# Kernel optimization log

Hardware: AMD Instinct MI355X
Metric: run time of the kernel (lower is better)

Reference implementation:

```python
import jax, jax.numpy as jnp
import numpy as np

N, T, H, W, C = 4, 8, 64, 64, 512
WS = 8  # window size; H, W are exact multiples so pad/depad are identity


def setup_inputs() -> dict:
    key = jax.random.key(0)
    k1, k2, k3, k4 = jax.random.split(key, 4)
    x = jax.random.normal(k1, (N, T, H, W, C), dtype=jnp.float32)
    local_pos_embed = jax.random.normal(k2, (WS, WS, C), dtype=jnp.float32)
    W_in = jax.random.normal(k3, (3 * C, C), dtype=jnp.float32) * 0.02
    b_in = jnp.zeros((3 * C,), dtype=jnp.float32)
    W_out = jax.random.normal(k4, (C, C), dtype=jnp.float32) * 0.02
    b_out = jnp.zeros((C,), dtype=jnp.float32)
    return {"x": x, "local_pos_embed": local_pos_embed, "W_in": W_in,
            "b_in": b_in, "W_out": W_out, "b_out": b_out, "num_heads": 8}


def reference(x, local_pos_embed, W_in, b_in, W_out, b_out, num_heads):
    n, t, h, w, c = x.shape
    ws = local_pos_embed.shape[0]
    nh, nw = h // ws, w // ws
    head_dim = c // num_heads
    scale = 1.0 / jnp.sqrt(jnp.asarray(head_dim, dtype=x.dtype))

    # window partition: (N*T, H, W, C) -> (N*T*nh*nw, ws*ws, C)
    xw = x.reshape(n * t, nh, ws, nw, ws, c)
    xw = xw.transpose(0, 1, 3, 2, 4, 5).reshape(n * t * nh * nw, ws * ws, c)

    pos = local_pos_embed.reshape(ws * ws, c)  # flatten(0,1)
    qk_in = xw + pos[None, :, :]               # pos added to q,k only

    Wq, Wk, Wv = W_in[:c], W_in[c:2 * c], W_in[2 * c:]
    bq, bk, bv = b_in[:c], b_in[c:2 * c], b_in[2 * c:]

    B, S = qk_in.shape[0], qk_in.shape[1]
    q = (qk_in @ Wq.T + bq).reshape(B, S, num_heads, head_dim)
    k = (qk_in @ Wk.T + bk).reshape(B, S, num_heads, head_dim)
    v = (xw @ Wv.T + bv).reshape(B, S, num_heads, head_dim)

    scores = jnp.einsum('bqhd,bkhd->bhqk', q * scale, k)
    attn = jax.nn.softmax(scores, axis=-1)
    out = jnp.einsum('bhqk,bkhd->bqhd', attn, v).reshape(B, S, c)
    out = out @ W_out.T + b_out

    # reverse window partition
    out = out.reshape(n * t, nh, nw, ws, ws, c)
    out = out.transpose(0, 1, 3, 2, 4, 5).reshape(n, t, h, w, c)
    return out
```

## Files before the change

kernel.cpp:

```cpp
#include <hip/hip_runtime.h>

typedef _Float16 f16;
typedef unsigned int u32;
typedef f16 f16x8 __attribute__((ext_vector_type(8)));
typedef f16 f16x4 __attribute__((ext_vector_type(4)));
typedef float f32x4 __attribute__((ext_vector_type(4)));


__device__ __forceinline__ int src_row(int m) {
    int win = m >> 6, s = m & 63;
    return ((win >> 6) << 12) | (((win >> 3) & 7) << 9) | ((s >> 3) << 6) |
           ((win & 7) << 3) | (s & 7);
}

__device__ __forceinline__ void gload_lds16(const void* g, void* lds) {
    __builtin_amdgcn_global_load_lds(
        (const __attribute__((address_space(1))) u32*)g,
        (__attribute__((address_space(3))) u32*)lds, 16, 0, 0);
}

__device__ __forceinline__ f16* sp(char* S, int r, int c) {
    return (f16*)(S + r * 1024 + ((c * 2) ^ ((r & 7) << 4)));
}

__global__ __launch_bounds__(256) void prep_weights_k(
        const float* __restrict__ Wi, const float* __restrict__ Wo,
        f16* __restrict__ Wi_h, f16* __restrict__ Wo_h) {
    int i = blockIdx.x * 256 + threadIdx.x;
    const float4* src;
    f16* dst;
    int idx;
    if (i < 196608) { src = (const float4*)Wi; dst = Wi_h; idx = i; }
    else            { src = (const float4*)Wo; dst = Wo_h; idx = i - 196608; }
    float4 v = src[idx];
    f16x4 h = {(f16)v.x, (f16)v.y, (f16)v.z, (f16)v.w};
    *(f16x4*)(dst + (size_t)idx * 4) = h;
}

__global__ __launch_bounds__(256) void prep_bias_k(
        const float* __restrict__ pos, const float* __restrict__ Wi,
        const float* __restrict__ b_in, float* __restrict__ biasT) {
    int idx = blockIdx.x * 256 + threadIdx.x;
    int s = idx / 1536, o = idx % 1536;
    float acc = b_in[o];
    if (o < 1024) {
        const float4* p4 = (const float4*)(pos + (size_t)s * 512);
        const float4* w4 = (const float4*)(Wi + (size_t)o * 512);
        #pragma unroll 4
        for (int c = 0; c < 128; ++c) {
            float4 a = p4[c], b = w4[c];
            acc += a.x * b.x + a.y * b.y + a.z * b.z + a.w * b.w;
        }
    }
    biasT[idx] = acc;
}

__global__ __launch_bounds__(256) void prep_x_k(
        const float* __restrict__ x, f16* __restrict__ xh, int m0) {
    int i = blockIdx.x * 256 + threadIdx.x;
    int ml = i >> 6, c8 = (i & 63) * 8;
    int sr = src_row(m0 + ml);
    const float4* s4 = (const float4*)(x + (size_t)sr * 512 + c8);
    float4 a = s4[0], b = s4[1];
    f16x8 hv = {(f16)a.x, (f16)a.y, (f16)a.z, (f16)a.w,
                (f16)b.x, (f16)b.y, (f16)b.z, (f16)b.w};
    *(f16x8*)(xh + (size_t)ml * 512 + c8) = hv;
}

__global__ void __launch_bounds__(512, 2) qkv_gemm8_k(
        const f16* __restrict__ xh, const f16* __restrict__ Wh,
        const float* __restrict__ biasT, f16* __restrict__ qkv, int nblk) {
    extern __shared__ f16 lds[];
    int tid = threadIdx.x;
    int lane = tid & 63, wid = tid >> 6;
    int l15 = lane & 15, g = lane >> 4;
    int wm = wid >> 2, wn = wid & 3;
    int sid = (blockIdx.x & 7) * (nblk >> 3) + (blockIdx.x >> 3);
    int bm = sid / 6, bn = sid % 6;
    const f16* Ap = xh + (size_t)bm * 256 * 512;
    const f16* Bp = Wh + (size_t)bn * 256 * 512;

    int li0 = tid, li1 = tid + 512;
    int r0 = li0 >> 3, c0 = li0 & 7, r1 = li1 >> 3, c1 = li1 & 7;
    int off0 = r0 * 512 + ((c0 ^ (r0 & 7)) * 8);
    int off1 = r1 * 512 + ((c1 ^ (r1 & 7)) * 8);

    auto stage = [&](const f16* panel, int ldsbase, int tt, int h) {
        int tb = tt & 1;
        int dst = ldsbase + (tb * 2 + h) * 8192 + wid * 512;
        const f16* src = panel + h * 65536 + tt * 64;
        gload_lds16(src + off0, (void*)&lds[dst]);
        gload_lds16(src + off1, (void*)&lds[dst + 4096]);
    };

    f32x4 acc[8][4];
    f32x4 zero4 = {0.f, 0.f, 0.f, 0.f};
    #pragma unroll
    for (int a = 0; a < 8; ++a)
        #pragma unroll
        for (int b = 0; b < 4; ++b) acc[a][b] = zero4;
    f16x8 bf[4][2];

    stage(Ap, 0, 0, 0); stage(Ap, 0, 0, 1);
    stage(Bp, 32768, 0, 0); stage(Bp, 32768, 0, 1);
    stage(Ap, 0, 1, 0); stage(Ap, 0, 1, 1);
    stage(Bp, 32768, 1, 0); stage(Bp, 32768, 1, 1);
    asm volatile("s_waitcnt vmcnt(0)" ::: "memory");
    __builtin_amdgcn_s_barrier();

    #pragma unroll
    for (int tt = 0; tt < 8; ++tt) {
        int tb = tt & 1;
        const f16* Ab = &lds[(tb * 2 + wm) * 8192];
        const f16* Bb = &lds[32768 + (tb * 2 + (wn >> 1)) * 8192];
        #pragma unroll
        for (int q = 0; q < 4; ++q) {
            f16x8 af[2][2];
            #pragma unroll
            for (int ml = 0; ml < 2; ++ml) {
                int rr = (q * 2 + ml) * 16 + l15;
                #pragma unroll
                for (int ks = 0; ks < 2; ++ks)
                    af[ml][ks] = *(const f16x8*)&Ab[rr * 64 + (((ks * 4 + g) ^ (rr & 7)) * 8)];
            }
            if (q == 0) {
                #pragma unroll
                for (int nf = 0; nf < 4; ++nf) {
                    int rb = (wn & 1) * 64 + nf * 16 + l15;
                    #pragma unroll
                    for (int ks = 0; ks < 2; ++ks)
                        bf[nf][ks] = *(const f16x8*)&Bb[rb * 64 + (((ks * 4 + g) ^ (rb & 7)) * 8)];
                }
            }
            if (q <= 1) {
                if ((tt & 1) ? (tt + 1 < 8) : (tt >= 2)) stage(Ap, 0, tt + 1, q);
            } else {
                if (tt + 2 < 8) stage(Bp, 32768, tt + 2, q - 2);
            }
            __builtin_amdgcn_s_barrier();
            __builtin_amdgcn_s_setprio(1);
            #pragma unroll
            for (int ml = 0; ml < 2; ++ml)
                #pragma unroll
                for (int nf = 0; nf < 4; ++nf)
                    #pragma unroll
                    for (int ks = 0; ks < 2; ++ks)
                        acc[q * 2 + ml][nf] = __builtin_amdgcn_mfma_f32_16x16x32_f16(
                            af[ml][ks], bf[nf][ks], acc[q * 2 + ml][nf], 0, 0, 0);
            __builtin_amdgcn_s_setprio(0);
            if (q == 3) {
                if (tt < 6)       asm volatile("s_waitcnt vmcnt(4)" ::: "memory");
                else if (tt == 6) asm volatile("s_waitcnt vmcnt(0)" ::: "memory");
            }
            __builtin_amdgcn_s_barrier();
        }
    }

    int browg = bm * 256 + wm * 128, bcolg = bn * 256 + wn * 64;
    #pragma unroll
    for (int mf = 0; mf < 8; ++mf) {
        #pragma unroll
        for (int nf = 0; nf < 4; ++nf) {
            int col = bcolg + nf * 16 + l15;
            #pragma unroll
            for (int j = 0; j < 4; ++j) {
                int row = browg + mf * 16 + g * 4 + j;
                float v = acc[mf][nf][j] + biasT[(row & 63) * 1536 + col];
                qkv[(size_t)row * 1536 + col] = (f16)v;
            }
        }
    }
}

__global__ __launch_bounds__(512) void attn_k(
        const f16* __restrict__ qkv, f16* __restrict__ attn_h) {
    __shared__ __align__(16) char S[64 * 1024];
    int tid = threadIdx.x;
    int lane = tid & 63, h = tid >> 6;
    int l15 = lane & 15, g = lane >> 4;
    const f16* base = qkv + (size_t)blockIdx.x * 64 * 1536;
    int qc = h * 64, kc = 512 + h * 64, vc = 1024 + h * 64;

    f32x4 zero4 = {0.f, 0.f, 0.f, 0.f};
    f32x4 acc[4][4];
    #pragma unroll
    for (int a = 0; a < 4; ++a)
        #pragma unroll
        for (int b = 0; b < 4; ++b) acc[a][b] = zero4;

    {
        f16x8 qf[4][2], kf[4][2];
        #pragma unroll
        for (int mf = 0; mf < 4; ++mf)
            #pragma unroll
            for (int ks = 0; ks < 2; ++ks)
                qf[mf][ks] = *reinterpret_cast<const f16x8*>(base + (size_t)(mf * 16 + l15) * 1536 + qc + ks * 32 + g * 8);
        #pragma unroll
        for (int nf = 0; nf < 4; ++nf)
            #pragma unroll
            for (int ks = 0; ks < 2; ++ks)
                kf[nf][ks] = *reinterpret_cast<const f16x8*>(base + (size_t)(nf * 16 + l15) * 1536 + kc + ks * 32 + g * 8);
        #pragma unroll
        for (int ks = 0; ks < 2; ++ks)
            #pragma unroll
            for (int mf = 0; mf < 4; ++mf)
                #pragma unroll
                for (int nf = 0; nf < 4; ++nf)
                    acc[mf][nf] = __builtin_amdgcn_mfma_f32_16x16x32_f16(qf[mf][ks], kf[nf][ks], acc[mf][nf], 0, 0, 0);
    }

    f16x8 vf[4][2];
    #pragma unroll
    for (int nf = 0; nf < 4; ++nf)
        #pragma unroll
        for (int ks = 0; ks < 2; ++ks) {
            f16x8 v;
            #pragma unroll
            for (int j = 0; j < 8; ++j)
                v[j] = base[(size_t)(ks * 32 + g * 8 + j) * 1536 + vc + nf * 16 + l15];
            vf[nf][ks] = v;
        }

    char* Sh = S + h * 8192;
    #pragma unroll
    for (int mf = 0; mf < 4; ++mf) {
        #pragma unroll
        for (int j = 0; j < 4; ++j) {
            float mx = -1e30f;
            #pragma unroll
            for (int nf = 0; nf < 4; ++nf) mx = fmaxf(mx, acc[mf][nf][j]);
            #pragma unroll
            for (int off = 1; off < 16; off <<= 1) mx = fmaxf(mx, __shfl_xor(mx, off));
            float e[4], sum = 0.f;
            #pragma unroll
            for (int nf = 0; nf < 4; ++nf) {
                e[nf] = __expf((acc[mf][nf][j] - mx) * 0.125f);
                sum += e[nf];
            }
            #pragma unroll
            for (int off = 1; off < 16; off <<= 1) sum += __shfl_xor(sum, off);
            float rinv = __fdividef(1.0f, sum);
            int row = mf * 16 + g * 4 + j;
            #pragma unroll
            for (int nf = 0; nf < 4; ++nf)
                *(f16*)(Sh + row * 128 + (((nf * 16 + l15) * 2) ^ ((row & 7) << 4))) = (f16)(e[nf] * rinv);
        }
    }

    f32x4 acc2[4][4];
    #pragma unroll
    for (int a = 0; a < 4; ++a)
        #pragma unroll
        for (int b = 0; b < 4; ++b) acc2[a][b] = zero4;
    #pragma unroll
    for (int ks = 0; ks < 2; ++ks)
        #pragma unroll
        for (int mf = 0; mf < 4; ++mf) {
            int rr = mf * 16 + l15;
            f16x8 pa = *reinterpret_cast<const f16x8*>(Sh + rr * 128 + (((ks * 32 + g * 8) * 2) ^ ((rr & 7) << 4)));
            #pragma unroll
            for (int nf = 0; nf < 4; ++nf)
                acc2[mf][nf] = __builtin_amdgcn_mfma_f32_16x16x32_f16(pa, vf[nf][ks], acc2[mf][nf], 0, 0, 0);
        }

    f16* dst = attn_h + (size_t)blockIdx.x * 64 * 512 + h * 64;
    #pragma unroll
    for (int mf = 0; mf < 4; ++mf)
        #pragma unroll
        for (int nf = 0; nf < 4; ++nf)
            #pragma unroll
            for (int j = 0; j < 4; ++j)
                dst[(size_t)(mf * 16 + g * 4 + j) * 512 + nf * 16 + l15] = (f16)acc2[mf][nf][j];
}

__global__ void __launch_bounds__(512, 2) proj_gemm8_k(
        const f16* __restrict__ attn_h, const f16* __restrict__ Woh,
        const float* __restrict__ b_out, float* __restrict__ out, int nblk, int m0) {
    extern __shared__ f16 lds[];
    int tid = threadIdx.x;
    int lane = tid & 63, wid = tid >> 6;
    int l15 = lane & 15, g = lane >> 4;
    int wm = wid >> 2, wn = wid & 3;
    int sid = (blockIdx.x & 7) * (nblk >> 3) + (blockIdx.x >> 3);
    int bm = sid >> 1, bn = sid & 1;
    const f16* Ap = attn_h + (size_t)bm * 256 * 512;
    const f16* Bp = Woh + (size_t)bn * 256 * 512;

    int li0 = tid, li1 = tid + 512;
    int r0 = li0 >> 3, c0 = li0 & 7, r1 = li1 >> 3, c1 = li1 & 7;
    int off0 = r0 * 512 + ((c0 ^ (r0 & 7)) * 8);
    int off1 = r1 * 512 + ((c1 ^ (r1 & 7)) * 8);

    auto stage = [&](const f16* panel, int ldsbase, int tt, int h) {
        int tb = tt & 1;
        int dst = ldsbase + (tb * 2 + h) * 8192 + wid * 512;
        const f16* src = panel + h * 65536 + tt * 64;
        gload_lds16(src + off0, (void*)&lds[dst]);
        gload_lds16(src + off1, (void*)&lds[dst + 4096]);
    };

    f32x4 acc[8][4];
    f32x4 zero4 = {0.f, 0.f, 0.f, 0.f};
    #pragma unroll
    for (int a = 0; a < 8; ++a)
        #pragma unroll
        for (int b = 0; b < 4; ++b) acc[a][b] = zero4;
    f16x8 bf[4][2];

    stage(Ap, 0, 0, 0); stage(Ap, 0, 0, 1);
    stage(Bp, 32768, 0, 0); stage(Bp, 32768, 0, 1);
    stage(Ap, 0, 1, 0); stage(Ap, 0, 1, 1);
    stage(Bp, 32768, 1, 0); stage(Bp, 32768, 1, 1);
    asm volatile("s_waitcnt vmcnt(0)" ::: "memory");
    __builtin_amdgcn_s_barrier();

    #pragma unroll
    for (int tt = 0; tt < 8; ++tt) {
        int tb = tt & 1;
        const f16* Ab = &lds[(tb * 2 + wm) * 8192];
        const f16* Bb = &lds[32768 + (tb * 2 + (wn >> 1)) * 8192];
        #pragma unroll
        for (int q = 0; q < 4; ++q) {
            f16x8 af[2][2];
            #pragma unroll
            for (int ml = 0; ml < 2; ++ml) {
                int rr = (q * 2 + ml) * 16 + l15;
                #pragma unroll
                for (int ks = 0; ks < 2; ++ks)
                    af[ml][ks] = *(const f16x8*)&Ab[rr * 64 + (((ks * 4 + g) ^ (rr & 7)) * 8)];
            }
            if (q == 0) {
                #pragma unroll
                for (int nf = 0; nf < 4; ++nf) {
                    int rb = (wn & 1) * 64 + nf * 16 + l15;
                    #pragma unroll
                    for (int ks = 0; ks < 2; ++ks)
                        bf[nf][ks] = *(const f16x8*)&Bb[rb * 64 + (((ks * 4 + g) ^ (rb & 7)) * 8)];
                }
            }
            if (q <= 1) {
                if ((tt & 1) ? (tt + 1 < 8) : (tt >= 2)) stage(Ap, 0, tt + 1, q);
            } else {
                if (tt + 2 < 8) stage(Bp, 32768, tt + 2, q - 2);
            }
            __builtin_amdgcn_s_barrier();
            __builtin_amdgcn_s_setprio(1);
            #pragma unroll
            for (int ml = 0; ml < 2; ++ml)
                #pragma unroll
                for (int nf = 0; nf < 4; ++nf)
                    #pragma unroll
                    for (int ks = 0; ks < 2; ++ks)
                        acc[q * 2 + ml][nf] = __builtin_amdgcn_mfma_f32_16x16x32_f16(
                            af[ml][ks], bf[nf][ks], acc[q * 2 + ml][nf], 0, 0, 0);
            __builtin_amdgcn_s_setprio(0);
            if (q == 3) {
                if (tt < 6)       asm volatile("s_waitcnt vmcnt(4)" ::: "memory");
                else if (tt == 6) asm volatile("s_waitcnt vmcnt(0)" ::: "memory");
            }
            __builtin_amdgcn_s_barrier();
        }
    }

    int browg = bm * 256 + wm * 128, bcolg = bn * 256 + wn * 64;
    #pragma unroll
    for (int nf = 0; nf < 4; ++nf) {
        int col = bcolg + nf * 16 + l15;
        float bo = b_out[col];
        #pragma unroll
        for (int mf = 0; mf < 8; ++mf) {
            #pragma unroll
            for (int j = 0; j < 4; ++j) {
                int srow = src_row(m0 + browg + mf * 16 + g * 4 + j);
                out[(size_t)srow * 512 + col] = acc[mf][nf][j] + bo;
            }
        }
    }
}

extern "C" void kernel_launch(void* const* d_in, const int* in_sizes, int n_in,
                              void* d_out, int out_size, void* d_ws, size_t ws_size,
                              hipStream_t stream) {
    (void)in_sizes; (void)n_in; (void)out_size;
    const float* x     = (const float*)d_in[0];
    const float* pos   = (const float*)d_in[1];
    const float* W_in  = (const float*)d_in[2];
    const float* b_in  = (const float*)d_in[3];
    const float* W_out = (const float*)d_in[4];
    const float* b_out = (const float*)d_in[5];
    float* out = (float*)d_out;

    char* ws = (char*)d_ws;
    f16*   Wi_h  = (f16*)ws;
    f16*   Wo_h  = (f16*)(ws + 1572864);
    float* biasT = (float*)(ws + 2097152);
    const size_t fixed = 2490368;

    int chunks = 1;
    while (chunks < 64) {
        size_t need = fixed + ((size_t)131072 / chunks) * 4096;
        if (need <= ws_size) break;
        chunks <<= 1;
    }
    int Mc = 131072 / chunks;
    f16* xh  = (f16*)(ws + fixed);
    f16* qkv = (f16*)(ws + fixed + (size_t)Mc * 1024);
    int nblk  = (Mc / 256) * 6;
    int nblk2 = (Mc / 256) * 2;

    static_cast<void>(hipFuncSetAttribute((const void*)qkv_gemm8_k,
        hipFuncAttributeMaxDynamicSharedMemorySize, 131072));
    static_cast<void>(hipFuncSetAttribute((const void*)proj_gemm8_k,
        hipFuncAttributeMaxDynamicSharedMemorySize, 131072));

    prep_weights_k<<<1024, 256, 0, stream>>>(W_in, W_out, Wi_h, Wo_h);
    prep_bias_k<<<384, 256, 0, stream>>>(pos, W_in, b_in, biasT);
    for (int c = 0; c < chunks; ++c) {
        int m0 = c * Mc;
        prep_x_k<<<Mc / 4, 256, 0, stream>>>(x, xh, m0);
        qkv_gemm8_k<<<nblk, 512, 131072, stream>>>(xh, Wi_h, biasT, qkv, nblk);
        attn_k<<<Mc / 64, 512, 0, stream>>>(qkv, xh);
        proj_gemm8_k<<<nblk2, 512, 131072, stream>>>(xh, Wo_h, b_out, out, nblk2, m0);
    }
}
```

Baseline: 635.0 us.

## Write V transposed per window/head from QKV GEMM epilogue and chunk into four

The QKV GEMM epilogue now splits its output into a Q/K buffer and a V buffer stored transposed per window and head, staged through LDS so the writes are vectorized. The attention kernel can then load V fragments with 16-byte vector loads instead of strided scalar gathers. The chunk count also starts at four, so each launch works on a smaller piece of the problem and the intermediates stay small enough to remain cache-resident. The cost is an extra LDS round trip and barriers in the V epilogue, plus four times as many kernel launches.

```diff
diff --git a/kernel.cpp b/kernel.cpp
--- a/kernel.cpp
+++ b/kernel.cpp
@@ -17,10 +17,6 @@
     __builtin_amdgcn_global_load_lds(
         (const __attribute__((address_space(1))) u32*)g,
         (__attribute__((address_space(3))) u32*)lds, 16, 0, 0);
-}
-
-__device__ __forceinline__ f16* sp(char* S, int r, int c) {
-    return (f16*)(S + r * 1024 + ((c * 2) ^ ((r & 7) << 4)));
 }
 
 __global__ __launch_bounds__(256) void prep_weights_k(
@@ -69,7 +65,8 @@
 
 __global__ void __launch_bounds__(512, 2) qkv_gemm8_k(
         const f16* __restrict__ xh, const f16* __restrict__ Wh,
-        const float* __restrict__ biasT, f16* __restrict__ qkv, int nblk) {
+        const float* __restrict__ biasT, f16* __restrict__ qk,
+        f16* __restrict__ vT, int nblk) {
     extern __shared__ f16 lds[];
     int tid = threadIdx.x;
     int lane = tid & 63, wid = tid >> 6;
@@ -156,30 +153,63 @@
         }
     }
 
-    int browg = bm * 256 + wm * 128, bcolg = bn * 256 + wn * 64;
-    #pragma unroll
-    for (int mf = 0; mf < 8; ++mf) {
-        #pragma unroll
-        for (int nf = 0; nf < 4; ++nf) {
-            int col = bcolg + nf * 16 + l15;
-            #pragma unroll
-            for (int j = 0; j < 4; ++j) {
-                int row = browg + mf * 16 + g * 4 + j;
-                float v = acc[mf][nf][j] + biasT[(row & 63) * 1536 + col];
-                qkv[(size_t)row * 1536 + col] = (f16)v;
-            }
+    int browg = bm * 256 + wm * 128;
+    if (bn < 4) {
+        #pragma unroll
+        for (int mf = 0; mf < 8; ++mf) {
+            #pragma unroll
+            for (int nf = 0; nf < 4; ++nf) {
+                int col = bn * 256 + wn * 64 + nf * 16 + l15;
+                #pragma unroll
+                for (int j = 0; j < 4; ++j) {
+                    int row = browg + mf * 16 + g * 4 + j;
+                    float v = acc[mf][nf][j] + biasT[(row & 63) * 1536 + col];
+                    qk[(size_t)row * 1024 + col] = (f16)v;
+                }
+            }
+        }
+    } else {
+        __syncthreads();
+        char* T = (char*)lds;
+        int bn2 = bn - 4;
+        #pragma unroll
+        for (int mf = 0; mf < 8; ++mf) {
+            #pragma unroll
+            for (int nf = 0; nf < 4; ++nf) {
+                int dl = wn * 64 + nf * 16 + l15;
+                float bo = biasT[1024 + bn2 * 256 + dl];
+                #pragma unroll
+                for (int j = 0; j < 4; ++j) {
+                    int sl = wm * 128 + mf * 16 + g * 4 + j;
+                    *(f16*)(T + dl * 512 + ((sl * 2) ^ ((dl & 7) << 4))) =
+                        (f16)(acc[mf][nf][j] + bo);
+                }
+            }
+        }
+        __syncthreads();
+        #pragma unroll
+        for (int r = 0; r < 16; ++r) {
+            int c = r * 512 + tid;
+            int dl = c >> 5, s0 = (c & 31) * 8;
+            f16x8 v = *(const f16x8*)(T + dl * 512 + ((s0 * 2) ^ ((dl & 7) << 4)));
+            int gcol = bn2 * 256 + dl;
+            int head = gcol >> 6, dd = gcol & 63;
+            int win = bm * 4 + (s0 >> 6);
+            *(f16x8*)(vT + (size_t)win * 32768 + head * 4096 + dd * 64 + (s0 & 63)) = v;
         }
     }
 }
 
 __global__ __launch_bounds__(512) void attn_k(
-        const f16* __restrict__ qkv, f16* __restrict__ attn_h) {
+        const f16* __restrict__ qk, const f16* __restrict__ vT,
+        f16* __restrict__ attn_h) {
     __shared__ __align__(16) char S[64 * 1024];
     int tid = threadIdx.x;
     int lane = tid & 63, h = tid >> 6;
     int l15 = lane & 15, g = lane >> 4;
-    const f16* base = qkv + (size_t)blockIdx.x * 64 * 1536;
-    int qc = h * 64, kc = 512 + h * 64, vc = 1024 + h * 64;
+    const f16* baseqk = qk + (size_t)blockIdx.x * 64 * 1024;
+    const f16* basev  = vT + (size_t)blockIdx.x * 32768 + h * 4096;
+    int qc = h * 64, kc = 512 + h * 64;
 
     f32x4 zero4 = {0.f, 0.f, 0.f, 0.f};
     f32x4 acc[4][4];
@@ -194,12 +224,12 @@
         for (int mf = 0; mf < 4; ++mf)
             #pragma unroll
             for (int ks = 0; ks < 2; ++ks)
-                qf[mf][ks] = *reinterpret_cast<const f16x8*>(base + (size_t)(mf * 16 + l15) * 1536 + qc + ks * 32 + g * 8);
+                qf[mf][ks] = *reinterpret_cast<const f16x8*>(baseqk + (size_t)(mf * 16 + l15) * 1024 + qc + ks * 32 + g * 8);
         #pragma unroll
         for (int nf = 0; nf < 4; ++nf)
             #pragma unroll
             for (int ks = 0; ks < 2; ++ks)
-                kf[nf][ks] = *reinterpret_cast<const f16x8*>(base + (size_t)(nf * 16 + l15) * 1536 + kc + ks * 32 + g * 8);
+                kf[nf][ks] = *reinterpret_cast<const f16x8*>(baseqk + (size_t)(nf * 16 + l15) * 1024 + kc + ks * 32 + g * 8);
         #pragma unroll
         for (int ks = 0; ks < 2; ++ks)
             #pragma unroll
@@ -213,13 +243,8 @@
     #pragma unroll
     for (int nf = 0; nf < 4; ++nf)
         #pragma unroll
-        for (int ks = 0; ks < 2; ++ks) {
-            f16x8 v;
-            #pragma unroll
-            for (int j = 0; j < 8; ++j)
-                v[j] = base[(size_t)(ks * 32 + g * 8 + j) * 1536 + vc + nf * 16 + l15];
-            vf[nf][ks] = v;
-        }
+        for (int ks = 0; ks < 2; ++ks)
+            vf[nf][ks] = *reinterpret_cast<const f16x8*>(basev + (nf * 16 + l15) * 64 + ks * 32 + g * 8);
 
     char* Sh = S + h * 8192;
     #pragma unroll
@@ -396,15 +421,16 @@
     float* biasT = (float*)(ws + 2097152);
     const size_t fixed = 2490368;
 
-    int chunks = 1;
+    int chunks = 4;
     while (chunks < 64) {
         size_t need = fixed + ((size_t)131072 / chunks) * 4096;
         if (need <= ws_size) break;
         chunks <<= 1;
     }
     int Mc = 131072 / chunks;
-    f16* xh  = (f16*)(ws + fixed);
-    f16* qkv = (f16*)(ws + fixed + (size_t)Mc * 1024);
+    f16* xh = (f16*)(ws + fixed);
+    f16* qk = (f16*)(ws + fixed + (size_t)Mc * 1024);
+    f16* vT = (f16*)(ws + fixed + (size_t)Mc * 3072);
     int nblk  = (Mc / 256) * 6;
     int nblk2 = (Mc / 256) * 2;
 
@@ -418,8 +444,8 @@
     for (int c = 0; c < chunks; ++c) {
         int m0 = c * Mc;
         prep_x_k<<<Mc / 4, 256, 0, stream>>>(x, xh, m0);
-        qkv_gemm8_k<<<nblk, 512, 131072, stream>>>(xh, Wi_h, biasT, qkv, nblk);
-        attn_k<<<Mc / 64, 512, 0, stream>>>(qkv, xh);
+        qkv_gemm8_k<<<nblk, 512, 131072, stream>>>(xh, Wi_h, biasT, qk, vT, nblk);
+        attn_k<<<Mc / 64, 512, 0, stream>>>(qk, vT, xh);
         proj_gemm8_k<<<nblk2, 512, 131072, stream>>>(xh, Wo_h, b_out, out, nblk2, m0);
     }
 }
```

After: 599.9 us. -5.5%, faster.
